# Kernel optimization log

Hardware: AMD Instinct MI355X
Metric: run time of the kernel (lower is better)

## Reference

```python
import jax, jax.numpy as jnp
import numpy as np

N = 50000       # nodes
E = 800000      # edges (avg degree 16)
C_IN = 128
C_OUT = 128
RATIO = 0.5
K = int(np.ceil(RATIO * N))  # static top-k size (single graph)
EPS = 1e-5      # BatchNorm eps


def setup_inputs() -> dict:
    key = jax.random.key(0)
    ks = jax.random.split(key, 12)
    x = jax.random.normal(ks[0], (N, C_IN), jnp.float32)
    edge_index = jax.random.randint(ks[1], (2, E), 0, N, dtype=jnp.int32)
    batch = jnp.zeros((N,), jnp.int32)
    s_in = 1.0 / np.sqrt(C_IN)
    s_out = 1.0 / np.sqrt(C_OUT)
    return {
        "x": x,
        "edge_index": edge_index,
        "batch": batch,
        "lin_w": jax.random.uniform(ks[2], (C_IN, C_OUT), jnp.float32, -s_in, s_in),
        "lin_b": jax.random.uniform(ks[3], (C_OUT,), jnp.float32, -s_in, s_in),
        "bn1_g": jnp.ones((C_OUT,), jnp.float32),
        "bn1_b": jnp.zeros((C_OUT,), jnp.float32),
        "gcn_w": jax.random.uniform(ks[4], (C_OUT, C_OUT), jnp.float32, -s_out, s_out),
        "gcn_b": jnp.zeros((C_OUT,), jnp.float32),
        "bn2_g": jnp.ones((C_OUT,), jnp.float32),
        "bn2_b": jnp.zeros((C_OUT,), jnp.float32),
        "pool_w": jax.random.uniform(ks[5], (C_OUT,), jnp.float32, -s_out, s_out),
    }


def _batchnorm(h, g, b):
    # training-mode BatchNorm1d: biased variance over the node axis
    mu = jnp.mean(h, axis=0)
    var = jnp.mean(jnp.square(h - mu), axis=0)
    return (h - mu) * jax.lax.rsqrt(var + EPS) * g + b


def reference(x, edge_index, batch, lin_w, lin_b, bn1_g, bn1_b,
              gcn_w, gcn_b, bn2_g, bn2_b, pool_w):
    # ---- MLP: Linear + BN + ReLU ----
    h = jax.nn.relu(_batchnorm(x @ lin_w + lin_b, bn1_g, bn1_b))

    # ---- GCNConv with self-loops + symmetric normalization ----
    loops = jnp.arange(N, dtype=edge_index.dtype)
    row = jnp.concatenate([edge_index[0], loops])  # source
    col = jnp.concatenate([edge_index[1], loops])  # target
    hw = h @ gcn_w                                    # [N, C_OUT]
    deg = jax.ops.segment_sum(jnp.ones_like(col, jnp.float32), col, num_segments=N)
    dinv = jnp.where(deg > 0, jax.lax.rsqrt(deg), 0.0)
    norm = dinv[row] * dinv[col]                      # [E+N]
    agg = jax.ops.segment_sum(hw[row] * norm[:, None], col, num_segments=N)
    out = agg + gcn_b

    # ---- BN + ReLU ----
    h2 = jax.nn.relu(_batchnorm(out, bn2_g, bn2_b))

    # ---- TopKPooling (single graph -> static k) ----
    score = jnp.tanh((h2 @ pool_w) / jnp.linalg.norm(pool_w))
    top_score, perm = jax.lax.top_k(score, K)
    x_pool = h2[perm] * top_score[:, None]            # [K, C_OUT]
    batch_new = batch[perm]

    # filter_adj with fixed shape: dropped edges marked -1
    mask = jnp.zeros((N,), bool).at[perm].set(True)
    new_idx = jnp.full((N,), -1, edge_index.dtype).at[perm].set(
        jnp.arange(K, dtype=edge_index.dtype))
    src, dst = edge_index[0], edge_index[1]
    keep = mask[src] & mask[dst]
    ei_new = jnp.where(keep[None, :],
                       jnp.stack([new_idx[src], new_idx[dst]]),
                       jnp.array(-1, edge_index.dtype))
    return x_pool, ei_new, batch_new
```

## Files before the change

kernel.cpp:

```cpp
#include <hip/hip_runtime.h>
#include <hip/hip_bf16.h>

#define NN 50000
#define EE 800000
#define KTOP 25000
#define EPSF 1e-5

__global__ __launch_bounds__(256, 2) void gemm_bn_stats(const float* __restrict__ A,
                                                        const float* __restrict__ W,
                                                        const float* __restrict__ bias,
                                                        float* __restrict__ Y,
                                                        double* __restrict__ part, int M) {
    __shared__ float Bs[128][128];
    __shared__ float As[32][128];
    int t = threadIdx.x;
    int bm = blockIdx.x * 128;

    const float4* W4 = (const float4*)W;
    float4* Bs4 = (float4*)Bs;
#pragma unroll
    for (int i = 0; i < 16; i++) Bs4[t + i * 256] = W4[t + i * 256];

    float acc[8][8];
#pragma unroll
    for (int i = 0; i < 8; i++)
#pragma unroll
        for (int j = 0; j < 8; j++) acc[i][j] = 0.f;

    int ty = t >> 4;
    int tx = t & 15;

    for (int kc = 0; kc < 4; kc++) {
        __syncthreads();
#pragma unroll
        for (int i = 0; i < 4; i++) {
            int f4 = t + i * 256;
            int r = f4 >> 3, k4 = f4 & 7;
            int row = bm + r;
            float4 v = make_float4(0.f, 0.f, 0.f, 0.f);
            if (row < M) v = *(const float4*)&A[(size_t)row * 128 + kc * 32 + k4 * 4];
            As[k4 * 4 + 0][r] = v.x;
            As[k4 * 4 + 1][r] = v.y;
            As[k4 * 4 + 2][r] = v.z;
            As[k4 * 4 + 3][r] = v.w;
        }
        __syncthreads();
#pragma unroll
        for (int kk = 0; kk < 32; kk++) {
            float4 a0 = *(float4*)&As[kk][ty * 8];
            float4 a1 = *(float4*)&As[kk][ty * 8 + 4];
            float4 b0 = *(float4*)&Bs[kc * 32 + kk][tx * 8];
            float4 b1 = *(float4*)&Bs[kc * 32 + kk][tx * 8 + 4];
            float av[8] = {a0.x, a0.y, a0.z, a0.w, a1.x, a1.y, a1.z, a1.w};
            float bv[8] = {b0.x, b0.y, b0.z, b0.w, b1.x, b1.y, b1.z, b1.w};
#pragma unroll
            for (int i = 0; i < 8; i++)
#pragma unroll
                for (int j = 0; j < 8; j++) acc[i][j] += av[i] * bv[j];
        }
    }

    float s[8], s2[8];
#pragma unroll
    for (int j = 0; j < 8; j++) { s[j] = 0.f; s2[j] = 0.f; }
#pragma unroll
    for (int i = 0; i < 8; i++) {
        int row = bm + ty * 8 + i;
        if (row < M) {
#pragma unroll
            for (int j = 0; j < 8; j++) {
                float yv = acc[i][j] + bias[tx * 8 + j];
                Y[(size_t)row * 128 + tx * 8 + j] = yv;
                s[j] += yv;
                s2[j] += yv * yv;
            }
        }
    }
    __syncthreads();
    float2* Sred = (float2*)As;
#pragma unroll
    for (int j = 0; j < 8; j++) Sred[ty * 128 + tx * 8 + j] = make_float2(s[j], s2[j]);
    __syncthreads();
    if (t < 128) {
        double S = 0.0, S2 = 0.0;
#pragma unroll
        for (int r = 0; r < 16; r++) {
            float2 v = Sred[r * 128 + t];
            S += (double)v.x;
            S2 += (double)v.y;
        }
        part[((size_t)blockIdx.x * 128 + t) * 2 + 0] = S;
        part[((size_t)blockIdx.x * 128 + t) * 2 + 1] = S2;
    }
}

__global__ __launch_bounds__(256, 2) void gemm_bn_apply(const float* __restrict__ Yin,
                                                        const float* __restrict__ W,
                                                        const float* __restrict__ sc,
                                                        const float* __restrict__ sh,
                                                        const float* __restrict__ dinv,
                                                        float* __restrict__ HWs, int M) {
    __shared__ float Bs[128][128];
    __shared__ float As[32][128];
    int t = threadIdx.x;
    int bm = blockIdx.x * 128;

    const float4* W4 = (const float4*)W;
    float4* Bs4 = (float4*)Bs;
#pragma unroll
    for (int i = 0; i < 16; i++) Bs4[t + i * 256] = W4[t + i * 256];

    float acc[8][8];
#pragma unroll
    for (int i = 0; i < 8; i++)
#pragma unroll
        for (int j = 0; j < 8; j++) acc[i][j] = 0.f;

    int ty = t >> 4;
    int tx = t & 15;

    for (int kc = 0; kc < 4; kc++) {
        __syncthreads();
#pragma unroll
        for (int i = 0; i < 4; i++) {
            int f4 = t + i * 256;
            int r = f4 >> 3, k4 = f4 & 7;
            int row = bm + r;
            int col = kc * 32 + k4 * 4;
            float4 v = make_float4(0.f, 0.f, 0.f, 0.f);
            if (row < M) {
                float4 y = *(const float4*)&Yin[(size_t)row * 128 + col];
                float4 scv = *(const float4*)&sc[col];
                float4 shv = *(const float4*)&sh[col];
                v.x = fmaxf(y.x * scv.x + shv.x, 0.f);
                v.y = fmaxf(y.y * scv.y + shv.y, 0.f);
                v.z = fmaxf(y.z * scv.z + shv.z, 0.f);
                v.w = fmaxf(y.w * scv.w + shv.w, 0.f);
            }
            As[k4 * 4 + 0][r] = v.x;
            As[k4 * 4 + 1][r] = v.y;
            As[k4 * 4 + 2][r] = v.z;
            As[k4 * 4 + 3][r] = v.w;
        }
        __syncthreads();
#pragma unroll
        for (int kk = 0; kk < 32; kk++) {
            float4 a0 = *(float4*)&As[kk][ty * 8];
            float4 a1 = *(float4*)&As[kk][ty * 8 + 4];
            float4 b0 = *(float4*)&Bs[kc * 32 + kk][tx * 8];
            float4 b1 = *(float4*)&Bs[kc * 32 + kk][tx * 8 + 4];
            float av[8] = {a0.x, a0.y, a0.z, a0.w, a1.x, a1.y, a1.z, a1.w};
            float bv[8] = {b0.x, b0.y, b0.z, b0.w, b1.x, b1.y, b1.z, b1.w};
#pragma unroll
            for (int i = 0; i < 8; i++)
#pragma unroll
                for (int j = 0; j < 8; j++) acc[i][j] += av[i] * bv[j];
        }
    }
#pragma unroll
    for (int i = 0; i < 8; i++) {
        int row = bm + ty * 8 + i;
        if (row < M) {
            float di = dinv[row];
#pragma unroll
            for (int j = 0; j < 8; j++)
                HWs[(size_t)row * 128 + tx * 8 + j] = acc[i][j] * di;
        }
    }
}

#define BN2_ROWS 64
#define BN2_NB ((NN + BN2_ROWS - 1) / BN2_ROWS)

__global__ __launch_bounds__(128) void bn_stats(const float* __restrict__ Y,
                                                double* __restrict__ part, int M) {
    int c = threadIdx.x;
    int b = blockIdx.x;
    int r0 = b * BN2_ROWS;
    int r1 = min(M, r0 + BN2_ROWS);
    double s = 0.0, s2 = 0.0;
    int r = r0;
    for (; r + 4 <= r1; r += 4) {
        float v0 = Y[(size_t)r * 128 + c];
        float v1 = Y[(size_t)(r + 1) * 128 + c];
        float v2 = Y[(size_t)(r + 2) * 128 + c];
        float v3 = Y[(size_t)(r + 3) * 128 + c];
        s += (double)v0 + (double)v1 + (double)v2 + (double)v3;
        s2 += (double)v0 * v0 + (double)v1 * v1 + (double)v2 * v2 + (double)v3 * v3;
    }
    for (; r < r1; r++) {
        float v = Y[(size_t)r * 128 + c];
        s += (double)v;
        s2 += (double)v * v;
    }
    part[((size_t)b * 128 + c) * 2 + 0] = s;
    part[((size_t)b * 128 + c) * 2 + 1] = s2;
}

__global__ __launch_bounds__(256) void bn_finalize(const double* __restrict__ part, int nb,
                                                   const float* __restrict__ g,
                                                   const float* __restrict__ beta,
                                                   float* __restrict__ scale,
                                                   float* __restrict__ shift, int M) {
    int c = blockIdx.x;
    int t = threadIdx.x;
    double s = 0.0, s2 = 0.0;
    for (int b = t; b < nb; b += 256) {
        s += part[((size_t)b * 128 + c) * 2 + 0];
        s2 += part[((size_t)b * 128 + c) * 2 + 1];
    }
    __shared__ double sd[256], sd2[256];
    sd[t] = s;
    sd2[t] = s2;
    __syncthreads();
#pragma unroll
    for (int o = 128; o > 0; o >>= 1) {
        if (t < o) {
            sd[t] += sd[t + o];
            sd2[t] += sd2[t + o];
        }
        __syncthreads();
    }
    if (t == 0) {
        double S = sd[0], S2 = sd2[0];
        double mu = S / (double)M;
        double var = S2 / (double)M - mu * mu;
        double inv = 1.0 / sqrt(var + (double)EPSF);
        scale[c] = (float)((double)g[c] * inv);
        shift[c] = (float)((double)beta[c] - mu * (double)g[c] * inv);
    }
}

__global__ __launch_bounds__(256) void count_deg(const int* __restrict__ col,
                                                 int* __restrict__ cnt, int E) {
    int e = blockIdx.x * 256 + threadIdx.x;
    if (e < E) atomicAdd(&cnt[col[e]], 1);
}

__global__ __launch_bounds__(256) void dinv_kernel(const int* __restrict__ cnt,
                                                   float* __restrict__ dinv, int M) {
    int i = blockIdx.x * 256 + threadIdx.x;
    if (i < M) {
        double deg = (double)(cnt[i] + 1);
        dinv[i] = (float)(1.0 / sqrt(deg));
    }
}

__global__ __launch_bounds__(256) void fill_csr(const int* __restrict__ row,
                                                const int* __restrict__ col,
                                                const int* __restrict__ off,
                                                int* __restrict__ cur,
                                                int* __restrict__ csr, int E) {
    int e = blockIdx.x * 256 + threadIdx.x;
    if (e < E) {
        int c = col[e];
        int p = atomicAdd(&cur[c], 1);
        csr[off[c] + p] = row[e];
    }
}

__device__ __forceinline__ int waveInclScan(int v, int lane) {
#pragma unroll
    for (int o = 1; o < 64; o <<= 1) {
        int u = __shfl_up(v, o, 64);
        if (lane >= o) v += u;
    }
    return v;
}

__global__ __launch_bounds__(1024) void scan_phase1(const int* __restrict__ in,
                                                    int* __restrict__ out,
                                                    int* __restrict__ bsum, int n) {
    int t = threadIdx.x;
    int g = blockIdx.x * 1024 + t;
    int lane = t & 63, wid = t >> 6;
    int v = (g < n) ? in[g] : 0;
    int incl = waveInclScan(v, lane);
    __shared__ int ws[16];
    if (lane == 63) ws[wid] = incl;
    __syncthreads();
    if (t < 16) {
        int x = ws[t];
#pragma unroll
        for (int o = 1; o < 16; o <<= 1) {
            int u = __shfl_up(x, o, 64);
            if (t >= o) x += u;
        }
        ws[t] = x;
    }
    __syncthreads();
    int pre = (wid > 0) ? ws[wid - 1] : 0;
    if (g < n) out[g] = pre + incl - v;
    if (t == 1023) bsum[blockIdx.x] = ws[15];
}

__global__ __launch_bounds__(1024) void scan_phase2(int* __restrict__ bsum, int B,
                                                    int* __restrict__ out, int n) {
    int t = threadIdx.x;
    int lane = t & 63, wid = t >> 6;
    int v = (t < B) ? bsum[t] : 0;
    int incl = waveInclScan(v, lane);
    __shared__ int ws[16];
    if (lane == 63) ws[wid] = incl;
    __syncthreads();
    if (t < 16) {
        int x = ws[t];
#pragma unroll
        for (int o = 1; o < 16; o <<= 1) {
            int u = __shfl_up(x, o, 64);
            if (t >= o) x += u;
        }
        ws[t] = x;
    }
    __syncthreads();
    int pre = (wid > 0) ? ws[wid - 1] : 0;
    int glob_incl = pre + incl;
    if (t < B) bsum[t] = glob_incl - v;
    if (t == B - 1) out[n] = glob_incl;
}

__global__ __launch_bounds__(1024) void scan_phase3(int* __restrict__ out,
                                                    const int* __restrict__ bsum, int n) {
    int g = blockIdx.x * 1024 + threadIdx.x;
    if (g < n) out[g] += bsum[blockIdx.x];
}

__global__ __launch_bounds__(256) void gcn_agg(const float* __restrict__ HWs,
                                               const int* __restrict__ off,
                                               const int* __restrict__ csr,
                                               const float* __restrict__ dinv,
                                               const float* __restrict__ gcn_b,
                                               float* __restrict__ OUT, int M) {
    int lane = threadIdx.x & 63;
    int i = blockIdx.x * 4 + (threadIdx.x >> 6);
    if (i >= M) return;
    const float2* H2 = (const float2*)HWs;
    int o0 = off[i], o1 = off[i + 1];
    float2 hv = H2[(size_t)i * 64 + lane];
    double ax = (double)hv.x, ay = (double)hv.y;
    int e = o0;
    for (; e + 4 <= o1; e += 4) {
        int s0 = csr[e], s1 = csr[e + 1], s2 = csr[e + 2], s3 = csr[e + 3];
        float2 v0 = H2[(size_t)s0 * 64 + lane];
        float2 v1 = H2[(size_t)s1 * 64 + lane];
        float2 v2 = H2[(size_t)s2 * 64 + lane];
        float2 v3 = H2[(size_t)s3 * 64 + lane];
        ax += (double)v0.x + (double)v1.x + (double)v2.x + (double)v3.x;
        ay += (double)v0.y + (double)v1.y + (double)v2.y + (double)v3.y;
    }
    for (; e < o1; e++) {
        float2 v = H2[(size_t)csr[e] * 64 + lane];
        ax += (double)v.x;
        ay += (double)v.y;
    }
    double di = (double)dinv[i];
    float2 ob = ((const float2*)gcn_b)[lane];
    float2 o;
    o.x = (float)(ax * di) + ob.x;
    o.y = (float)(ay * di) + ob.y;
    ((float2*)OUT)[(size_t)i * 64 + lane] = o;
}

__global__ __launch_bounds__(256) void score_key(const float* __restrict__ Y2,
                                                 const float* __restrict__ sc,
                                                 const float* __restrict__ sh,
                                                 const float* __restrict__ w,
                                                 float* __restrict__ score,
                                                 unsigned* __restrict__ key,
                                                 int* __restrict__ bcnt, int M) {
    int lane = threadIdx.x & 63;
    int wid = threadIdx.x >> 6;
    int gw = blockIdx.x * 4 + wid;
    int nw = gridDim.x * 4;

    float w0 = w[lane], w1 = w[lane + 64];
    float sc0 = sc[lane], sh0 = sh[lane];
    float sc1 = sc[lane + 64], sh1 = sh[lane + 64];

    float nv = w0 * w0 + w1 * w1;
#pragma unroll
    for (int o = 32; o >= 1; o >>= 1) nv += __shfl_xor(nv, o, 64);
    float nrm = sqrtf(nv);

    for (int r = gw; r < M; r += nw) {
        float a = Y2[(size_t)r * 128 + lane];
        float b = Y2[(size_t)r * 128 + lane + 64];
        a = fmaxf(a * sc0 + sh0, 0.f);
        b = fmaxf(b * sc1 + sh1, 0.f);
        float v = a * w0 + b * w1;
#pragma unroll
        for (int o = 32; o >= 1; o >>= 1) v += __shfl_xor(v, o, 64);
        if (lane == 0) {
            float s = tanhf(v / nrm);
            score[r] = s;
            unsigned u = __float_as_uint(s);
            unsigned k = (u & 0x80000000u) ? ~u : (u | 0x80000000u);
            key[r] = k;
            atomicAdd(&bcnt[k >> 16], 1);
        }
    }
}

__global__ __launch_bounds__(256) void bucket_fill(const unsigned* __restrict__ key,
                                                   const int* __restrict__ boff,
                                                   int* __restrict__ bcur,
                                                   int* __restrict__ bmem, int M) {
    int i = blockIdx.x * 256 + threadIdx.x;
    if (i < M) {
        int b = key[i] >> 16;
        int p = atomicAdd(&bcur[b], 1);
        bmem[boff[b] + p] = i;
    }
}

__global__ __launch_bounds__(256) void rank_kernel(const unsigned* __restrict__ key,
                                                   const int* __restrict__ boff,
                                                   const int* __restrict__ bmem,
                                                   int* __restrict__ rank,
                                                   int* __restrict__ nidx, int M) {
    int i = blockIdx.x * 256 + threadIdx.x;
    if (i >= M) return;
    unsigned ki = key[i];
    int b = ki >> 16;
    int r = M - boff[b + 1];
    int p0 = boff[b], p1 = boff[b + 1];
    for (int p = p0; p < p1; p++) {
        int j = bmem[p];
        unsigned kj = key[j];
        if (kj > ki || (kj == ki && j < i)) r++;
    }
    rank[i] = r;
    nidx[i] = (r < KTOP) ? r : -1;
}

__global__ __launch_bounds__(128) void write_pool(const float* __restrict__ Y2,
                                                  const float* __restrict__ sc,
                                                  const float* __restrict__ sh,
                                                  const float* __restrict__ score,
                                                  const int* __restrict__ rank,
                                                  float* __restrict__ out0,
                                                  float* __restrict__ out2, int M) {
    int i = blockIdx.x;
    int c = threadIdx.x;
    int r = rank[i];
    if (r < KTOP) {
        float h = fmaxf(Y2[(size_t)i * 128 + c] * sc[c] + sh[c], 0.f);
        out0[(size_t)r * 128 + c] = h * score[i];
        if (c == 0) out2[r] = 0.0f;
    }
}

__global__ __launch_bounds__(256) void write_edges(const int* __restrict__ row,
                                                   const int* __restrict__ col,
                                                   const int* __restrict__ nidx,
                                                   float* __restrict__ out1, int E) {
    int e = blockIdx.x * 256 + threadIdx.x;
    if (e < E) {
        int a = nidx[row[e]];
        int b = nidx[col[e]];
        bool keep = (a >= 0) && (b >= 0);
        out1[e] = keep ? (float)a : -1.0f;
        out1[E + e] = keep ? (float)b : -1.0f;
    }
}

extern "C" void kernel_launch(void* const* d_in, const int* in_sizes, int n_in,
                              void* d_out, int out_size, void* d_ws, size_t ws_size,
                              hipStream_t stream) {
    const float* x = (const float*)d_in[0];
    const int* ei = (const int*)d_in[1];
    const float* lin_w = (const float*)d_in[3];
    const float* lin_b = (const float*)d_in[4];
    const float* bn1_g = (const float*)d_in[5];
    const float* bn1_b = (const float*)d_in[6];
    const float* gcn_w = (const float*)d_in[7];
    const float* gcn_b = (const float*)d_in[8];
    const float* bn2_g = (const float*)d_in[9];
    const float* bn2_b = (const float*)d_in[10];
    const float* pool_w = (const float*)d_in[11];

    const int* e_row = ei;
    const int* e_col = ei + EE;

    char* ws = (char*)d_ws;
    size_t off_b = 0;
    auto alloc = [&](size_t bytes) -> void* {
        void* p = ws + off_b;
        off_b = (off_b + bytes + 255) & ~(size_t)255;
        return p;
    };
    float* y = (float*)alloc((size_t)NN * 128 * 4);
    float* hws = (float*)alloc((size_t)NN * 128 * 4);
    int* cnt = (int*)alloc(NN * 4);
    int* cur = (int*)alloc(NN * 4);
    int* offs = (int*)alloc((NN + 1) * 4);
    float* dinv = (float*)alloc(NN * 4);
    int* csr = (int*)alloc((size_t)EE * 4);
    float* score = (float*)alloc(NN * 4);
    unsigned* key = (unsigned*)alloc(NN * 4);
    int* rank = (int*)alloc(NN * 4);
    int* nidx = (int*)alloc(NN * 4);
    int* bcnt = (int*)alloc(65536 * 4);
    int* boff = (int*)alloc((65536 + 1) * 4);
    int* bcur = (int*)alloc(65536 * 4);
    int* bmem = (int*)alloc(NN * 4);
    double* part = (double*)alloc((size_t)BN2_NB * 128 * 2 * 8);
    float* scale1 = (float*)alloc(128 * 4);
    float* shift1 = (float*)alloc(128 * 4);
    float* scale2 = (float*)alloc(128 * 4);
    float* shift2 = (float*)alloc(128 * 4);
    int* bsum = (int*)alloc(128 * 4);

    float* out0 = (float*)d_out;
    float* out1 = out0 + (size_t)KTOP * 128;
    float* out2 = out1 + (size_t)2 * EE;

    int gemm_grid = (NN + 127) / 128;

    hipMemsetAsync(cnt, 0, NN * 4, stream);
    hipMemsetAsync(cur, 0, NN * 4, stream);
    hipMemsetAsync(bcnt, 0, 65536 * 4, stream);
    hipMemsetAsync(bcur, 0, 65536 * 4, stream);
    count_deg<<<(EE + 255) / 256, 256, 0, stream>>>(e_col, cnt, EE);
    dinv_kernel<<<(NN + 255) / 256, 256, 0, stream>>>(cnt, dinv, NN);
    {
        int B = (NN + 1023) / 1024;
        scan_phase1<<<B, 1024, 0, stream>>>(cnt, offs, bsum, NN);
        scan_phase2<<<1, 1024, 0, stream>>>(bsum, B, offs, NN);
        scan_phase3<<<B, 1024, 0, stream>>>(offs, bsum, NN);
    }
    fill_csr<<<(EE + 255) / 256, 256, 0, stream>>>(e_row, e_col, offs, cur, csr, EE);

    gemm_bn_stats<<<gemm_grid, 256, 0, stream>>>(x, lin_w, lin_b, y, part, NN);
    bn_finalize<<<128, 256, 0, stream>>>(part, gemm_grid, bn1_g, bn1_b, scale1, shift1, NN);

    gemm_bn_apply<<<gemm_grid, 256, 0, stream>>>(y, gcn_w, scale1, shift1, dinv, hws, NN);
    gcn_agg<<<(NN + 3) / 4, 256, 0, stream>>>(hws, offs, csr, dinv, gcn_b, y, NN);

    bn_stats<<<BN2_NB, 128, 0, stream>>>(y, part, NN);
    bn_finalize<<<128, 256, 0, stream>>>(part, BN2_NB, bn2_g, bn2_b, scale2, shift2, NN);

    score_key<<<512, 256, 0, stream>>>(y, scale2, shift2, pool_w, score, key, bcnt, NN);
    {
        int B = 65536 / 1024;
        scan_phase1<<<B, 1024, 0, stream>>>(bcnt, boff, bsum, 65536);
        scan_phase2<<<1, 1024, 0, stream>>>(bsum, B, boff, 65536);
        scan_phase3<<<B, 1024, 0, stream>>>(boff, bsum, 65536);
    }
    bucket_fill<<<(NN + 255) / 256, 256, 0, stream>>>(key, boff, bcur, bmem, NN);
    rank_kernel<<<(NN + 255) / 256, 256, 0, stream>>>(key, boff, bmem, rank, nidx, NN);

    write_pool<<<NN, 128, 0, stream>>>(y, scale2, shift2, score, rank, out0, out2, NN);
    write_edges<<<(EE + 255) / 256, 256, 0, stream>>>(e_row, e_col, nidx, out1, EE);
}
```

Baseline: 381.7 us.

## Vectorize GEMM epilogues and pool writes, fuse dinv into scan, unroll gather

```diff
diff --git a/kernel.cpp b/kernel.cpp
--- a/kernel.cpp
+++ b/kernel.cpp
@@ -12,7 +12,7 @@
                                                         float* __restrict__ Y,
                                                         double* __restrict__ part, int M) {
     __shared__ float Bs[128][128];
-    __shared__ float As[32][128];
+    __shared__ float As[32][132];
     int t = threadIdx.x;
     int bm = blockIdx.x * 128;
 
@@ -49,8 +49,8 @@
         for (int kk = 0; kk < 32; kk++) {
             float4 a0 = *(float4*)&As[kk][ty * 8];
             float4 a1 = *(float4*)&As[kk][ty * 8 + 4];
-            float4 b0 = *(float4*)&Bs[kc * 32 + kk][tx * 8];
-            float4 b1 = *(float4*)&Bs[kc * 32 + kk][tx * 8 + 4];
+            float4 b0 = *(float4*)&Bs[kc * 32 + kk][tx * 4];
+            float4 b1 = *(float4*)&Bs[kc * 32 + kk][64 + tx * 4];
             float av[8] = {a0.x, a0.y, a0.z, a0.w, a1.x, a1.y, a1.z, a1.w};
             float bv[8] = {b0.x, b0.y, b0.z, b0.w, b1.x, b1.y, b1.z, b1.w};
 #pragma unroll
@@ -60,6 +60,8 @@
         }
     }
 
+    float4 bb0 = *(const float4*)&bias[tx * 4];
+    float4 bb1 = *(const float4*)&bias[64 + tx * 4];
     float s[8], s2[8];
 #pragma unroll
     for (int j = 0; j < 8; j++) { s[j] = 0.f; s2[j] = 0.f; }
@@ -67,19 +69,30 @@
     for (int i = 0; i < 8; i++) {
         int row = bm + ty * 8 + i;
         if (row < M) {
-#pragma unroll
-            for (int j = 0; j < 8; j++) {
-                float yv = acc[i][j] + bias[tx * 8 + j];
-                Y[(size_t)row * 128 + tx * 8 + j] = yv;
-                s[j] += yv;
-                s2[j] += yv * yv;
-            }
+            float4 y0, y1;
+            y0.x = acc[i][0] + bb0.x; y0.y = acc[i][1] + bb0.y;
+            y0.z = acc[i][2] + bb0.z; y0.w = acc[i][3] + bb0.w;
+            y1.x = acc[i][4] + bb1.x; y1.y = acc[i][5] + bb1.y;
+            y1.z = acc[i][6] + bb1.z; y1.w = acc[i][7] + bb1.w;
+            *(float4*)&Y[(size_t)row * 128 + tx * 4] = y0;
+            *(float4*)&Y[(size_t)row * 128 + 64 + tx * 4] = y1;
+            s[0] += y0.x; s2[0] += y0.x * y0.x;
+            s[1] += y0.y; s2[1] += y0.y * y0.y;
+            s[2] += y0.z; s2[2] += y0.z * y0.z;
+            s[3] += y0.w; s2[3] += y0.w * y0.w;
+            s[4] += y1.x; s2[4] += y1.x * y1.x;
+            s[5] += y1.y; s2[5] += y1.y * y1.y;
+            s[6] += y1.z; s2[6] += y1.z * y1.z;
+            s[7] += y1.w; s2[7] += y1.w * y1.w;
         }
     }
     __syncthreads();
     float2* Sred = (float2*)As;
 #pragma unroll
-    for (int j = 0; j < 8; j++) Sred[ty * 128 + tx * 8 + j] = make_float2(s[j], s2[j]);
+    for (int j = 0; j < 8; j++) {
+        int col = (j < 4) ? (tx * 4 + j) : (64 + tx * 4 + j - 4);
+        Sred[ty * 128 + col] = make_float2(s[j], s2[j]);
+    }
     __syncthreads();
     if (t < 128) {
         double S = 0.0, S2 = 0.0;
@@ -101,7 +114,7 @@
                                                         const float* __restrict__ dinv,
                                                         float* __restrict__ HWs, int M) {
     __shared__ float Bs[128][128];
-    __shared__ float As[32][128];
+    __shared__ float As[32][132];
     int t = threadIdx.x;
     int bm = blockIdx.x * 128;
 
@@ -147,8 +160,8 @@
         for (int kk = 0; kk < 32; kk++) {
             float4 a0 = *(float4*)&As[kk][ty * 8];
             float4 a1 = *(float4*)&As[kk][ty * 8 + 4];
-            float4 b0 = *(float4*)&Bs[kc * 32 + kk][tx * 8];
-            float4 b1 = *(float4*)&Bs[kc * 32 + kk][tx * 8 + 4];
+            float4 b0 = *(float4*)&Bs[kc * 32 + kk][tx * 4];
+            float4 b1 = *(float4*)&Bs[kc * 32 + kk][64 + tx * 4];
             float av[8] = {a0.x, a0.y, a0.z, a0.w, a1.x, a1.y, a1.z, a1.w};
             float bv[8] = {b0.x, b0.y, b0.z, b0.w, b1.x, b1.y, b1.z, b1.w};
 #pragma unroll
@@ -162,9 +175,13 @@
         int row = bm + ty * 8 + i;
         if (row < M) {
             float di = dinv[row];
-#pragma unroll
-            for (int j = 0; j < 8; j++)
-                HWs[(size_t)row * 128 + tx * 8 + j] = acc[i][j] * di;
+            float4 o0, o1;
+            o0.x = acc[i][0] * di; o0.y = acc[i][1] * di;
+            o0.z = acc[i][2] * di; o0.w = acc[i][3] * di;
+            o1.x = acc[i][4] * di; o1.y = acc[i][5] * di;
+            o1.z = acc[i][6] * di; o1.w = acc[i][7] * di;
+            *(float4*)&HWs[(size_t)row * 128 + tx * 4] = o0;
+            *(float4*)&HWs[(size_t)row * 128 + 64 + tx * 4] = o1;
         }
     }
 }
@@ -237,15 +254,6 @@
     if (e < E) atomicAdd(&cnt[col[e]], 1);
 }
 
-__global__ __launch_bounds__(256) void dinv_kernel(const int* __restrict__ cnt,
-                                                   float* __restrict__ dinv, int M) {
-    int i = blockIdx.x * 256 + threadIdx.x;
-    if (i < M) {
-        double deg = (double)(cnt[i] + 1);
-        dinv[i] = (float)(1.0 / sqrt(deg));
-    }
-}
-
 __global__ __launch_bounds__(256) void fill_csr(const int* __restrict__ row,
                                                 const int* __restrict__ col,
                                                 const int* __restrict__ off,
@@ -270,11 +278,13 @@
 
 __global__ __launch_bounds__(1024) void scan_phase1(const int* __restrict__ in,
                                                     int* __restrict__ out,
-                                                    int* __restrict__ bsum, int n) {
+                                                    int* __restrict__ bsum,
+                                                    float* __restrict__ dinv, int n) {
     int t = threadIdx.x;
     int g = blockIdx.x * 1024 + t;
     int lane = t & 63, wid = t >> 6;
     int v = (g < n) ? in[g] : 0;
+    if (dinv && g < n) dinv[g] = (float)(1.0 / sqrt((double)(v + 1)));
     int incl = waveInclScan(v, lane);
     __shared__ int ws[16];
     if (lane == 63) ws[wid] = incl;
@@ -339,14 +349,21 @@
     float2 hv = H2[(size_t)i * 64 + lane];
     double ax = (double)hv.x, ay = (double)hv.y;
     int e = o0;
-    for (; e + 4 <= o1; e += 4) {
+    for (; e + 8 <= o1; e += 8) {
         int s0 = csr[e], s1 = csr[e + 1], s2 = csr[e + 2], s3 = csr[e + 3];
+        int s4 = csr[e + 4], s5 = csr[e + 5], s6 = csr[e + 6], s7 = csr[e + 7];
         float2 v0 = H2[(size_t)s0 * 64 + lane];
         float2 v1 = H2[(size_t)s1 * 64 + lane];
         float2 v2 = H2[(size_t)s2 * 64 + lane];
         float2 v3 = H2[(size_t)s3 * 64 + lane];
-        ax += (double)v0.x + (double)v1.x + (double)v2.x + (double)v3.x;
-        ay += (double)v0.y + (double)v1.y + (double)v2.y + (double)v3.y;
+        float2 v4 = H2[(size_t)s4 * 64 + lane];
+        float2 v5 = H2[(size_t)s5 * 64 + lane];
+        float2 v6 = H2[(size_t)s6 * 64 + lane];
+        float2 v7 = H2[(size_t)s7 * 64 + lane];
+        ax += ((double)v0.x + (double)v1.x) + ((double)v2.x + (double)v3.x) +
+              ((double)v4.x + (double)v5.x) + ((double)v6.x + (double)v7.x);
+        ay += ((double)v0.y + (double)v1.y) + ((double)v2.y + (double)v3.y) +
+              ((double)v4.y + (double)v5.y) + ((double)v6.y + (double)v7.y);
     }
     for (; e < o1; e++) {
         float2 v = H2[(size_t)csr[e] * 64 + lane];
@@ -391,9 +408,8 @@
 #pragma unroll
         for (int o = 32; o >= 1; o >>= 1) v += __shfl_xor(v, o, 64);
         if (lane == 0) {
-            float s = tanhf(v / nrm);
-            score[r] = s;
-            unsigned u = __float_as_uint(s);
+            score[r] = tanhf(v / nrm);
+            unsigned u = __float_as_uint(v);
             unsigned k = (u & 0x80000000u) ? ~u : (u | 0x80000000u);
             key[r] = k;
             atomicAdd(&bcnt[k >> 16], 1);
@@ -440,13 +456,23 @@
                                                   const int* __restrict__ rank,
                                                   float* __restrict__ out0,
                                                   float* __restrict__ out2, int M) {
-    int i = blockIdx.x;
-    int c = threadIdx.x;
+    int sub = threadIdx.x >> 5;
+    int c4 = threadIdx.x & 31;
+    int i = blockIdx.x * 4 + sub;
+    if (i >= M) return;
     int r = rank[i];
     if (r < KTOP) {
-        float h = fmaxf(Y2[(size_t)i * 128 + c] * sc[c] + sh[c], 0.f);
-        out0[(size_t)r * 128 + c] = h * score[i];
-        if (c == 0) out2[r] = 0.0f;
+        float s = score[i];
+        float4 y = *(const float4*)&Y2[(size_t)i * 128 + c4 * 4];
+        float4 scv = *(const float4*)&sc[c4 * 4];
+        float4 shv = *(const float4*)&sh[c4 * 4];
+        float4 o;
+        o.x = fmaxf(y.x * scv.x + shv.x, 0.f) * s;
+        o.y = fmaxf(y.y * scv.y + shv.y, 0.f) * s;
+        o.z = fmaxf(y.z * scv.z + shv.z, 0.f) * s;
+        o.w = fmaxf(y.w * scv.w + shv.w, 0.f) * s;
+        *(float4*)&out0[(size_t)r * 128 + c4 * 4] = o;
+        if (c4 == 0) out2[r] = 0.0f;
     }
 }
 
@@ -522,10 +548,9 @@
     hipMemsetAsync(bcnt, 0, 65536 * 4, stream);
     hipMemsetAsync(bcur, 0, 65536 * 4, stream);
     count_deg<<<(EE + 255) / 256, 256, 0, stream>>>(e_col, cnt, EE);
-    dinv_kernel<<<(NN + 255) / 256, 256, 0, stream>>>(cnt, dinv, NN);
     {
         int B = (NN + 1023) / 1024;
-        scan_phase1<<<B, 1024, 0, stream>>>(cnt, offs, bsum, NN);
+        scan_phase1<<<B, 1024, 0, stream>>>(cnt, offs, bsum, dinv, NN);
         scan_phase2<<<1, 1024, 0, stream>>>(bsum, B, offs, NN);
         scan_phase3<<<B, 1024, 0, stream>>>(offs, bsum, NN);
     }
@@ -543,13 +568,13 @@
     score_key<<<512, 256, 0, stream>>>(y, scale2, shift2, pool_w, score, key, bcnt, NN);
     {
         int B = 65536 / 1024;
-        scan_phase1<<<B, 1024, 0, stream>>>(bcnt, boff, bsum, 65536);
+        scan_phase1<<<B, 1024, 0, stream>>>(bcnt, boff, bsum, nullptr, 65536);
         scan_phase2<<<1, 1024, 0, stream>>>(bsum, B, boff, 65536);
         scan_phase3<<<B, 1024, 0, stream>>>(boff, bsum, 65536);
     }
     bucket_fill<<<(NN + 255) / 256, 256, 0, stream>>>(key, boff, bcur, bmem, NN);
     rank_kernel<<<(NN + 255) / 256, 256, 0, stream>>>(key, boff, bmem, rank, nidx, NN);
 
-    write_pool<<<NN, 128, 0, stream>>>(y, scale2, shift2, score, rank, out0, out2, NN);
+    write_pool<<<(NN + 3) / 4, 128, 0, stream>>>(y, scale2, shift2, score, rank, out0, out2, NN);
     write_edges<<<(EE + 255) / 256, 256, 0, stream>>>(e_row, e_col, nidx, out1, EE);
 }
```

New measurement: 363.0 us. 4.9% less time.
